# Performance work log

Hardware: AMD Instinct MI355X
Metric: run time of the kernel (lower is better)

## Reference

```python
import jax, jax.numpy as jnp
import numpy as np


def _pairwise_smooth_l1_sum(x):
    # x: [N, D]. All N^2 ordered pairs (i, j), including i == j (diff = 0),
    # matching torch's full index_select over [i for i ... for j ...].
    d = x[:, None, :] - x[None, :, :]            # [N, N, D]
    ad = jnp.abs(d)
    # SmoothL1 with beta = 1 (torch default): 0.5*d^2 if |d| < 1 else |d| - 0.5
    sl1 = jnp.where(ad < 1.0, 0.5 * d * d, ad - 0.5)
    return jnp.sum(sl1, axis=-1).reshape(-1)     # [N*N]


def setup_inputs() -> dict:
    key = jax.random.key(0)
    k1, k2 = jax.random.split(key)
    N, D = 512, 512
    teacher = jax.random.normal(k1, (N, D), dtype=jnp.float32)
    student = jax.random.normal(k2, (N, D), dtype=jnp.float32)
    return {"teacher": teacher, "student": student}


def reference(teacher, student):
    teacher_l2s = _pairwise_smooth_l1_sum(teacher)
    teacher_l2s = teacher_l2s / jnp.mean(teacher_l2s)
    student_l2s = _pairwise_smooth_l1_sum(student)
    student_l2s = student_l2s / jnp.mean(student_l2s)
    return jnp.sum(jnp.abs(teacher_l2s - student_l2s))
```

## Files before the change

kernel.cpp:

```cpp
#include <hip/hip_runtime.h>

#define N 512
#define D 512
#define TILE 32
#define DC 64
#define PITCH 68
#define NT 16
#define NTILES 136
#define NSLICE 8

__device__ __forceinline__ void sl1(float& acc, float x, float y) {
    float d  = x - y;
    float ad = fabsf(d);
    float m  = fminf(ad, 1.0f);
    acc = fmaf(m, fmaf(2.0f, ad, -m), acc);
}


__global__ __launch_bounds__(256, 8) void pair_sums_kernel(
    const float* __restrict__ Tm, const float* __restrict__ Sm,
    float* __restrict__ Pp, float* __restrict__ sums)
{
    const int mat = blockIdx.z;
    const int sl  = blockIdx.y;
    const float* __restrict__ X = mat ? Sm : Tm;
    float* __restrict__ Pm = Pp + (size_t)(mat * NSLICE + sl) * (N * N);

    int rem = blockIdx.x, ti = 0;
    while (rem >= NT - ti) { rem -= NT - ti; ++ti; }
    const int tj = ti + rem;
    const int i0 = ti * TILE, j0 = tj * TILE;
    const int d0 = sl * DC;

    __shared__ float Xi[TILE][PITCH];
    __shared__ float Xj[TILE][PITCH];

    const int t  = threadIdx.x;
    const int tx = t & 15;
    const int ty = t >> 4;

    #pragma unroll
    for (int kk = 0; kk < 2; ++kk) {
        int idx = t + kk * 256;
        int row = idx >> 4;
        int c4  = (idx & 15) * 4;
        *(float4*)&Xi[row][c4] = *(const float4*)&X[(size_t)(i0 + row) * D + d0 + c4];
        *(float4*)&Xj[row][c4] = *(const float4*)&X[(size_t)(j0 + row) * D + d0 + c4];
    }
    __syncthreads();

    float a00 = 0.f, a01 = 0.f, a10 = 0.f, a11 = 0.f;
    #pragma unroll 4
    for (int d4 = 0; d4 < DC / 4; ++d4) {
        float4 p0 = *(const float4*)&Xi[ty][d4 * 4];
        float4 p1 = *(const float4*)&Xi[ty + 16][d4 * 4];
        float4 q0 = *(const float4*)&Xj[tx][d4 * 4];
        float4 q1 = *(const float4*)&Xj[tx + 16][d4 * 4];
        sl1(a00, p0.x, q0.x); sl1(a00, p0.y, q0.y); sl1(a00, p0.z, q0.z); sl1(a00, p0.w, q0.w);
        sl1(a01, p0.x, q1.x); sl1(a01, p0.y, q1.y); sl1(a01, p0.z, q1.z); sl1(a01, p0.w, q1.w);
        sl1(a10, p1.x, q0.x); sl1(a10, p1.y, q0.y); sl1(a10, p1.z, q0.z); sl1(a10, p1.w, q0.w);
        sl1(a11, p1.x, q1.x); sl1(a11, p1.y, q1.y); sl1(a11, p1.z, q1.z); sl1(a11, p1.w, q1.w);
    }

    const bool diag = (ti == tj);
    const bool w00 = !diag || (ty <= tx);
    const bool w10 = !diag;
    const float s00 = 0.5f * a00, s01 = 0.5f * a01, s10 = 0.5f * a10, s11 = 0.5f * a11;

    float bs = 0.f;
    if (w00) { Pm[(i0 + ty     ) * N + (j0 + tx     )] = s00; bs += s00; }
              { Pm[(i0 + ty     ) * N + (j0 + tx + 16)] = s01; bs += s01; }
    if (w10) { Pm[(i0 + ty + 16) * N + (j0 + tx     )] = s10; bs += s10; }
    if (w00) { Pm[(i0 + ty + 16) * N + (j0 + tx + 16)] = s11; bs += s11; }

    #pragma unroll
    for (int off = 32; off > 0; off >>= 1) bs += __shfl_down(bs, off, 64);
    __shared__ float wpart[4];
    if ((t & 63) == 0) wpart[t >> 6] = bs;
    __syncthreads();
    if (t == 0) atomicAdd(&sums[mat], wpart[0] + wpart[1] + wpart[2] + wpart[3]);
}

__global__ __launch_bounds__(256) void final_kernel(
    const float* __restrict__ Pp, const float* __restrict__ sums, float* __restrict__ out)
{
    const float NN = (float)N * (float)N;
    const float cT = NN / (2.0f * sums[0]);
    const float cS = NN / (2.0f * sums[1]);
    float local = 0.0f;
    const int nvec = N * N / 4;
    for (int v = blockIdx.x * 256 + threadIdx.x; v < nvec; v += gridDim.x * 256) {
        int i  = v >> 7;
        int jb = (v & 127) * 4;
        if (jb + 3 < i) continue;
        float4 tq = make_float4(0.f, 0.f, 0.f, 0.f);
        float4 sq = make_float4(0.f, 0.f, 0.f, 0.f);
        #pragma unroll
        for (int s = 0; s < NSLICE; ++s) {
            float4 a = ((const float4*)(Pp + (size_t)s * (N * N)))[v];
            float4 b = ((const float4*)(Pp + (size_t)(NSLICE + s) * (N * N)))[v];
            tq.x += a.x; tq.y += a.y; tq.z += a.z; tq.w += a.w;
            sq.x += b.x; sq.y += b.y; sq.z += b.z; sq.w += b.w;
        }
        if (jb + 0 >= i) local += fabsf(tq.x * cT - sq.x * cS);
        if (jb + 1 >= i) local += fabsf(tq.y * cT - sq.y * cS);
        if (jb + 2 >= i) local += fabsf(tq.z * cT - sq.z * cS);
        if (jb + 3 >= i) local += fabsf(tq.w * cT - sq.w * cS);
    }
    #pragma unroll
    for (int off = 32; off > 0; off >>= 1) local += __shfl_down(local, off, 64);
    __shared__ float wpart[4];
    if ((threadIdx.x & 63) == 0) wpart[threadIdx.x >> 6] = local;
    __syncthreads();
    if (threadIdx.x == 0) atomicAdd(out, 2.0f * (wpart[0] + wpart[1] + wpart[2] + wpart[3]));
}

extern "C" void kernel_launch(void* const* d_in, const int* in_sizes, int n_in,
                              void* d_out, int out_size, void* d_ws, size_t ws_size,
                              hipStream_t stream) {
    const float* teacher = (const float*)d_in[0];
    const float* student = (const float*)d_in[1];
    float* out  = (float*)d_out;
    float* Pp   = (float*)d_ws;
    float* sums = Pp + (size_t)2 * NSLICE * N * N;

    hipMemsetAsync(sums, 0, 2 * sizeof(float), stream);
    hipMemsetAsync(d_out, 0, sizeof(float), stream);

    dim3 grid(NTILES, NSLICE, 2);
    pair_sums_kernel<<<grid, 256, 0, stream>>>(teacher, student, Pp, sums);
    final_kernel<<<256, 256, 0, stream>>>(Pp, sums, out);
}
```

Measured before the change: 97.87 us.

## Halve D-slices per block and loop over chunks to cut partial-sum traffic

Each block now processes two 64-wide D chunks in sequence, so the number of slices (and thus partial N×N buffers written and re-read) drops from 8 to 4 per matrix. The pair kernel stores all four outputs unconditionally and masks only the block sum, and the final kernel launches one thread per float4 instead of a grid-stride loop. This reduces workspace write/read bandwidth and final-kernel work, at the cost of fewer blocks (less parallelism) and an extra barrier per block.

After: 85.03 us. 13.1% less time.

```diff
diff --git a/kernel.cpp b/kernel.cpp
--- a/kernel.cpp
+++ b/kernel.cpp
@@ -7,7 +7,8 @@
 #define PITCH 68
 #define NT 16
 #define NTILES 136
-#define NSLICE 8
+#define NSLICE 4
+#define CHUNKS 2
 
 __device__ __forceinline__ void sl1(float& acc, float x, float y) {
     float d  = x - y;
@@ -30,7 +31,6 @@
     while (rem >= NT - ti) { rem -= NT - ti; ++ti; }
     const int tj = ti + rem;
     const int i0 = ti * TILE, j0 = tj * TILE;
-    const int d0 = sl * DC;
 
     __shared__ float Xi[TILE][PITCH];
     __shared__ float Xj[TILE][PITCH];
@@ -39,39 +39,46 @@
     const int tx = t & 15;
     const int ty = t >> 4;
 
-    #pragma unroll
-    for (int kk = 0; kk < 2; ++kk) {
-        int idx = t + kk * 256;
-        int row = idx >> 4;
-        int c4  = (idx & 15) * 4;
-        *(float4*)&Xi[row][c4] = *(const float4*)&X[(size_t)(i0 + row) * D + d0 + c4];
-        *(float4*)&Xj[row][c4] = *(const float4*)&X[(size_t)(j0 + row) * D + d0 + c4];
-    }
-    __syncthreads();
+    float a00 = 0.f, a01 = 0.f, a10 = 0.f, a11 = 0.f;
 
-    float a00 = 0.f, a01 = 0.f, a10 = 0.f, a11 = 0.f;
-    #pragma unroll 4
-    for (int d4 = 0; d4 < DC / 4; ++d4) {
-        float4 p0 = *(const float4*)&Xi[ty][d4 * 4];
-        float4 p1 = *(const float4*)&Xi[ty + 16][d4 * 4];
-        float4 q0 = *(const float4*)&Xj[tx][d4 * 4];
-        float4 q1 = *(const float4*)&Xj[tx + 16][d4 * 4];
-        sl1(a00, p0.x, q0.x); sl1(a00, p0.y, q0.y); sl1(a00, p0.z, q0.z); sl1(a00, p0.w, q0.w);
-        sl1(a01, p0.x, q1.x); sl1(a01, p0.y, q1.y); sl1(a01, p0.z, q1.z); sl1(a01, p0.w, q1.w);
-        sl1(a10, p1.x, q0.x); sl1(a10, p1.y, q0.y); sl1(a10, p1.z, q0.z); sl1(a10, p1.w, q0.w);
-        sl1(a11, p1.x, q1.x); sl1(a11, p1.y, q1.y); sl1(a11, p1.z, q1.z); sl1(a11, p1.w, q1.w);
+    for (int c = 0; c < CHUNKS; ++c) {
+        const int d0 = (sl * CHUNKS + c) * DC;
+        if (c) __syncthreads();
+        #pragma unroll
+        for (int kk = 0; kk < 2; ++kk) {
+            int idx = t + kk * 256;
+            int row = idx >> 4;
+            int c4  = (idx & 15) * 4;
+            *(float4*)&Xi[row][c4] = *(const float4*)&X[(size_t)(i0 + row) * D + d0 + c4];
+            *(float4*)&Xj[row][c4] = *(const float4*)&X[(size_t)(j0 + row) * D + d0 + c4];
+        }
+        __syncthreads();
+        #pragma unroll
+        for (int d4 = 0; d4 < DC / 4; ++d4) {
+            float4 p0 = *(const float4*)&Xi[ty][d4 * 4];
+            float4 p1 = *(const float4*)&Xi[ty + 16][d4 * 4];
+            float4 q0 = *(const float4*)&Xj[tx][d4 * 4];
+            float4 q1 = *(const float4*)&Xj[tx + 16][d4 * 4];
+            sl1(a00, p0.x, q0.x); sl1(a00, p0.y, q0.y); sl1(a00, p0.z, q0.z); sl1(a00, p0.w, q0.w);
+            sl1(a01, p0.x, q1.x); sl1(a01, p0.y, q1.y); sl1(a01, p0.z, q1.z); sl1(a01, p0.w, q1.w);
+            sl1(a10, p1.x, q0.x); sl1(a10, p1.y, q0.y); sl1(a10, p1.z, q0.z); sl1(a10, p1.w, q0.w);
+            sl1(a11, p1.x, q1.x); sl1(a11, p1.y, q1.y); sl1(a11, p1.z, q1.z); sl1(a11, p1.w, q1.w);
+        }
     }
 
-    const bool diag = (ti == tj);
-    const bool w00 = !diag || (ty <= tx);
-    const bool w10 = !diag;
     const float s00 = 0.5f * a00, s01 = 0.5f * a01, s10 = 0.5f * a10, s11 = 0.5f * a11;
 
-    float bs = 0.f;
-    if (w00) { Pm[(i0 + ty     ) * N + (j0 + tx     )] = s00; bs += s00; }
-              { Pm[(i0 + ty     ) * N + (j0 + tx + 16)] = s01; bs += s01; }
-    if (w10) { Pm[(i0 + ty + 16) * N + (j0 + tx     )] = s10; bs += s10; }
-    if (w00) { Pm[(i0 + ty + 16) * N + (j0 + tx + 16)] = s11; bs += s11; }
+    Pm[(i0 + ty     ) * N + (j0 + tx     )] = s00;
+    Pm[(i0 + ty     ) * N + (j0 + tx + 16)] = s01;
+    Pm[(i0 + ty + 16) * N + (j0 + tx     )] = s10;
+    Pm[(i0 + ty + 16) * N + (j0 + tx + 16)] = s11;
+
+    float bs;
+    if (ti == tj) {
+        bs = (ty <= tx ? s00 + s11 : 0.f) + s01;
+    } else {
+        bs = s00 + s01 + s10 + s11;
+    }
 
     #pragma unroll
     for (int off = 32; off > 0; off >>= 1) bs += __shfl_down(bs, off, 64);
@@ -87,12 +94,13 @@
     const float NN = (float)N * (float)N;
     const float cT = NN / (2.0f * sums[0]);
     const float cS = NN / (2.0f * sums[1]);
+
+    const int v  = blockIdx.x * 256 + threadIdx.x;
+    const int i  = v >> 7;
+    const int jb = (v & 127) * 4;
+
     float local = 0.0f;
-    const int nvec = N * N / 4;
-    for (int v = blockIdx.x * 256 + threadIdx.x; v < nvec; v += gridDim.x * 256) {
-        int i  = v >> 7;
-        int jb = (v & 127) * 4;
-        if (jb + 3 < i) continue;
+    if (jb + 3 >= i) {
         float4 tq = make_float4(0.f, 0.f, 0.f, 0.f);
         float4 sq = make_float4(0.f, 0.f, 0.f, 0.f);
         #pragma unroll
@@ -107,6 +115,7 @@
         if (jb + 2 >= i) local += fabsf(tq.z * cT - sq.z * cS);
         if (jb + 3 >= i) local += fabsf(tq.w * cT - sq.w * cS);
     }
+
     #pragma unroll
     for (int off = 32; off > 0; off >>= 1) local += __shfl_down(local, off, 64);
     __shared__ float wpart[4];
@@ -129,5 +138,5 @@
 
     dim3 grid(NTILES, NSLICE, 2);
     pair_sums_kernel<<<grid, 256, 0, stream>>>(teacher, student, Pp, sums);
-    final_kernel<<<256, 256, 0, stream>>>(Pp, sums, out);
+    final_kernel<<<N * N / 4 / 256, 256, 0, stream>>>(Pp, sums, out);
 }
```

## Accumulate slice partials atomically into one plane and enlarge pair tiles

Applied to the files above, without the earlier changes.

Each block now covers a 64x64 pair tile with a 4x4 register micro-tile per thread, and the feature chunk is split into 16 slices instead of 8. Slices no longer write separate per-slice partial planes. They atomically add into a single zeroed N×N plane per matrix, so the final kernel reads only two planes with one float4 per thread, and a last-block counter writes the output. This is meant to cut the large partial-plane write and readback traffic. The cost is many contended float atomics to L2, a 2 MB memset each call, and fewer blocks with higher register pressure.

After: 222.0 us. +126.9%, slower.

```diff
diff --git a/kernel.cpp b/kernel.cpp
--- a/kernel.cpp
+++ b/kernel.cpp
@@ -2,12 +2,12 @@
 
 #define N 512
 #define D 512
-#define TILE 32
-#define DC 64
-#define PITCH 68
-#define NT 16
-#define NTILES 136
-#define NSLICE 8
+#define TILE 64
+#define DC 32
+#define PITCH 36
+#define NT 8
+#define NTILES 36
+#define NSLICE 16
 
 __device__ __forceinline__ void sl1(float& acc, float x, float y) {
     float d  = x - y;
@@ -16,15 +16,16 @@
     acc = fmaf(m, fmaf(2.0f, ad, -m), acc);
 }
 
+#define ZONE_FLOATS (2 * N * N + 4)
 
-__global__ __launch_bounds__(256, 8) void pair_sums_kernel(
+__global__ __launch_bounds__(256, 4) void pair_sums_kernel(
     const float* __restrict__ Tm, const float* __restrict__ Sm,
     float* __restrict__ Pp, float* __restrict__ sums)
 {
     const int mat = blockIdx.z;
     const int sl  = blockIdx.y;
     const float* __restrict__ X = mat ? Sm : Tm;
-    float* __restrict__ Pm = Pp + (size_t)(mat * NSLICE + sl) * (N * N);
+    float* __restrict__ Pm = Pp + (size_t)mat * (N * N);
 
     int rem = blockIdx.x, ti = 0;
     while (rem >= NT - ti) { rem -= NT - ti; ++ti; }
@@ -42,36 +43,50 @@
     #pragma unroll
     for (int kk = 0; kk < 2; ++kk) {
         int idx = t + kk * 256;
-        int row = idx >> 4;
-        int c4  = (idx & 15) * 4;
+        int row = idx >> 3;
+        int c4  = (idx & 7) * 4;
         *(float4*)&Xi[row][c4] = *(const float4*)&X[(size_t)(i0 + row) * D + d0 + c4];
         *(float4*)&Xj[row][c4] = *(const float4*)&X[(size_t)(j0 + row) * D + d0 + c4];
     }
     __syncthreads();
 
-    float a00 = 0.f, a01 = 0.f, a10 = 0.f, a11 = 0.f;
-    #pragma unroll 4
+    float acc[4][4];
+    #pragma unroll
+    for (int m = 0; m < 4; ++m)
+        #pragma unroll
+        for (int n = 0; n < 4; ++n) acc[m][n] = 0.f;
+
+    #pragma unroll
     for (int d4 = 0; d4 < DC / 4; ++d4) {
-        float4 p0 = *(const float4*)&Xi[ty][d4 * 4];
-        float4 p1 = *(const float4*)&Xi[ty + 16][d4 * 4];
-        float4 q0 = *(const float4*)&Xj[tx][d4 * 4];
-        float4 q1 = *(const float4*)&Xj[tx + 16][d4 * 4];
-        sl1(a00, p0.x, q0.x); sl1(a00, p0.y, q0.y); sl1(a00, p0.z, q0.z); sl1(a00, p0.w, q0.w);
-        sl1(a01, p0.x, q1.x); sl1(a01, p0.y, q1.y); sl1(a01, p0.z, q1.z); sl1(a01, p0.w, q1.w);
-        sl1(a10, p1.x, q0.x); sl1(a10, p1.y, q0.y); sl1(a10, p1.z, q0.z); sl1(a10, p1.w, q0.w);
-        sl1(a11, p1.x, q1.x); sl1(a11, p1.y, q1.y); sl1(a11, p1.z, q1.z); sl1(a11, p1.w, q1.w);
+        float4 p[4], q[4];
+        #pragma unroll
+        for (int m = 0; m < 4; ++m) p[m] = *(const float4*)&Xi[ty + 16 * m][d4 * 4];
+        #pragma unroll
+        for (int n = 0; n < 4; ++n) q[n] = *(const float4*)&Xj[tx + 16 * n][d4 * 4];
+        #pragma unroll
+        for (int m = 0; m < 4; ++m)
+            #pragma unroll
+            for (int n = 0; n < 4; ++n) {
+                sl1(acc[m][n], p[m].x, q[n].x);
+                sl1(acc[m][n], p[m].y, q[n].y);
+                sl1(acc[m][n], p[m].z, q[n].z);
+                sl1(acc[m][n], p[m].w, q[n].w);
+            }
     }
 
     const bool diag = (ti == tj);
-    const bool w00 = !diag || (ty <= tx);
-    const bool w10 = !diag;
-    const float s00 = 0.5f * a00, s01 = 0.5f * a01, s10 = 0.5f * a10, s11 = 0.5f * a11;
-
     float bs = 0.f;
-    if (w00) { Pm[(i0 + ty     ) * N + (j0 + tx     )] = s00; bs += s00; }
-              { Pm[(i0 + ty     ) * N + (j0 + tx + 16)] = s01; bs += s01; }
-    if (w10) { Pm[(i0 + ty + 16) * N + (j0 + tx     )] = s10; bs += s10; }
-    if (w00) { Pm[(i0 + ty + 16) * N + (j0 + tx + 16)] = s11; bs += s11; }
+    #pragma unroll
+    for (int m = 0; m < 4; ++m)
+        #pragma unroll
+        for (int n = 0; n < 4; ++n) {
+            const int li = ty + 16 * m, lj = tx + 16 * n;
+            const float s = 0.5f * acc[m][n];
+            if (!diag || (li <= lj)) {
+                atomicAdd(&Pm[(i0 + li) * N + (j0 + lj)], s);
+                bs += s;
+            }
+        }
 
     #pragma unroll
     for (int off = 32; off > 0; off >>= 1) bs += __shfl_down(bs, off, 64);
@@ -82,37 +97,36 @@
 }
 
 __global__ __launch_bounds__(256) void final_kernel(
-    const float* __restrict__ Pp, const float* __restrict__ sums, float* __restrict__ out)
+    const float* __restrict__ Pp, float* __restrict__ sums, float* __restrict__ out)
 {
+    float* fin = sums + 2;
+    unsigned int* cnt = (unsigned int*)(sums + 3);
+
     const float NN = (float)N * (float)N;
     const float cT = NN / (2.0f * sums[0]);
     const float cS = NN / (2.0f * sums[1]);
-    float local = 0.0f;
-    const int nvec = N * N / 4;
-    for (int v = blockIdx.x * 256 + threadIdx.x; v < nvec; v += gridDim.x * 256) {
-        int i  = v >> 7;
-        int jb = (v & 127) * 4;
-        if (jb + 3 < i) continue;
-        float4 tq = make_float4(0.f, 0.f, 0.f, 0.f);
-        float4 sq = make_float4(0.f, 0.f, 0.f, 0.f);
-        #pragma unroll
-        for (int s = 0; s < NSLICE; ++s) {
-            float4 a = ((const float4*)(Pp + (size_t)s * (N * N)))[v];
-            float4 b = ((const float4*)(Pp + (size_t)(NSLICE + s) * (N * N)))[v];
-            tq.x += a.x; tq.y += a.y; tq.z += a.z; tq.w += a.w;
-            sq.x += b.x; sq.y += b.y; sq.z += b.z; sq.w += b.w;
-        }
-        if (jb + 0 >= i) local += fabsf(tq.x * cT - sq.x * cS);
-        if (jb + 1 >= i) local += fabsf(tq.y * cT - sq.y * cS);
-        if (jb + 2 >= i) local += fabsf(tq.z * cT - sq.z * cS);
-        if (jb + 3 >= i) local += fabsf(tq.w * cT - sq.w * cS);
-    }
+
+    const int v = blockIdx.x * 256 + threadIdx.x;
+    float4 tq = ((const float4*)Pp)[v];
+    float4 sq = ((const float4*)(Pp + (size_t)N * N))[v];
+    float local = fabsf(tq.x * cT - sq.x * cS) + fabsf(tq.y * cT - sq.y * cS)
+                + fabsf(tq.z * cT - sq.z * cS) + fabsf(tq.w * cT - sq.w * cS);
+
     #pragma unroll
     for (int off = 32; off > 0; off >>= 1) local += __shfl_down(local, off, 64);
     __shared__ float wpart[4];
     if ((threadIdx.x & 63) == 0) wpart[threadIdx.x >> 6] = local;
     __syncthreads();
-    if (threadIdx.x == 0) atomicAdd(out, 2.0f * (wpart[0] + wpart[1] + wpart[2] + wpart[3]));
+
+    if (threadIdx.x == 0) {
+        atomicAdd(fin, wpart[0] + wpart[1] + wpart[2] + wpart[3]);
+        __threadfence();
+        unsigned int old = atomicAdd(cnt, 1u);
+        if (old == gridDim.x - 1) {
+            float tot = atomicAdd(fin, 0.0f);
+            out[0] = 2.0f * tot;
+        }
+    }
 }
 
 extern "C" void kernel_launch(void* const* d_in, const int* in_sizes, int n_in,
@@ -122,12 +136,11 @@
     const float* student = (const float*)d_in[1];
     float* out  = (float*)d_out;
     float* Pp   = (float*)d_ws;
-    float* sums = Pp + (size_t)2 * NSLICE * N * N;
+    float* sums = Pp + 2 * (size_t)N * N;
 
-    hipMemsetAsync(sums, 0, 2 * sizeof(float), stream);
-    hipMemsetAsync(d_out, 0, sizeof(float), stream);
+    hipMemsetAsync(d_ws, 0, ZONE_FLOATS * sizeof(float), stream);
 
     dim3 grid(NTILES, NSLICE, 2);
     pair_sums_kernel<<<grid, 256, 0, stream>>>(teacher, student, Pp, sums);
-    final_kernel<<<256, 256, 0, stream>>>(Pp, sums, out);
+    final_kernel<<<N * N / 4 / 256, 256, 0, stream>>>(Pp, sums, out);
 }
```
